# Kernel optimization log

Measured on AMD Instinct MI355X. Metric: run time of the kernel, lower is better.

Reference implementation:

```python
import jax, jax.numpy as jnp
import numpy as np

B, S, D, H = 4, 1024, 1024, 16
DH = D // H
NEG = -10000.0  # mask fill value for non-float32 (bool) masks in the torch code


def setup_inputs() -> dict:
    key = jax.random.key(0)
    ks = jax.random.split(key, 16)
    scale = 0.02
    inp = {
        "query": jax.random.normal(ks[0], (B, S, D), jnp.float32),
        "key": jax.random.normal(ks[1], (B, S, D), jnp.float32),
        "value": jax.random.normal(ks[2], (B, S, D), jnp.float32),
        "pos_embedding": jax.random.normal(ks[3], (B, S, D), jnp.float32),
        # learned params (torch Linear convention: y = x @ W.T + b, W is (out,in))
        "Wq": jax.random.normal(ks[4], (D, D), jnp.float32) * scale,
        "bq": jnp.zeros((D,), jnp.float32),
        "Wk": jax.random.normal(ks[5], (D, D), jnp.float32) * scale,
        "bk": jnp.zeros((D,), jnp.float32),
        "Wv": jax.random.normal(ks[6], (D, D), jnp.float32) * scale,
        "bv": jnp.zeros((D,), jnp.float32),
        "Wpos": jax.random.normal(ks[7], (D, D), jnp.float32) * scale,
        "u_bias": jax.random.normal(ks[8], (H, DH), jnp.float32) * scale,
        "v_bias": jax.random.normal(ks[9], (H, DH), jnp.float32) * scale,
        "Wout": jax.random.normal(ks[10], (D, D), jnp.float32) * scale,
        "bout": jnp.zeros((D,), jnp.float32),
    }
    # right-padding mask: lengths in [S//2, S]; mask[b,i,j] = pad(i) | pad(j)
    lengths = jax.random.randint(ks[11], (B,), S // 2, S + 1)
    pad = jnp.arange(S)[None, :] >= lengths[:, None]  # (B,S)
    inp["mask"] = pad[:, :, None] | pad[:, None, :]  # (B,S,S) bool
    return inp


def _relative_shift(pos_score, mask):
    """Batch-safe Transformer-XL relative shift (vectorized version of the
    per-batch python loop). pos_score: (B,H,S,S), mask: (B,S,S) bool."""
    b, h, s, _ = pos_score.shape
    # per-row true length: S - number of padded rows (column 0 is never padded)
    L = s - jnp.sum(mask[:, :, 0].astype(jnp.int32), axis=-1)  # (B,)
    i = jnp.arange(s)[:, None]
    j = jnp.arange(s)[None, :]

    def shift_one(ps, Lb):  # ps: (H,S,S), Lb: scalar int
        # padded[h,r,0]=0; padded[h,r,k]=ps[h,r,k-1]; flat index of out[i,j] in
        # the (Lb+1, Lb) reshape of padded[:, :Lb, :Lb+1], rows 1: -> offset Lb
        m = Lb + i * Lb + j            # (S,S)
        row = m // (Lb + 1)
        col = m % (Lb + 1)
        g = ps[:, jnp.clip(row, 0, s - 1), jnp.clip(col - 1, 0, s - 1)]  # (H,S,S)
        valid = (i < Lb) & (j < Lb) & (col != 0)
        return jnp.where(valid[None], g, jnp.zeros((), ps.dtype))

    shifted = jax.vmap(shift_one)(pos_score, L)
    # masked_fill_(padding_mask, 0.0)
    return jnp.where(mask[:, None, :, :], jnp.zeros((), pos_score.dtype), shifted)


def reference(query, key, value, pos_embedding, mask,
              Wq, bq, Wk, bk, Wv, bv, Wpos, u_bias, v_bias, Wout, bout):
    b = query.shape[0]
    sqrt_dim = np.sqrt(D).astype(np.float32)

    q = (query @ Wq.T + bq).reshape(b, -1, H, DH)                 # (B,S,H,dh)
    k = (key @ Wk.T + bk).reshape(b, -1, H, DH)                   # (B,S,H,dh)
    v = (value @ Wv.T + bv).reshape(b, -1, H, DH)                 # (B,S,H,dh)
    p = (pos_embedding @ Wpos.T).reshape(b, -1, H, DH)            # (B,S,H,dh)

    content_score = jnp.einsum('bqhd,bkhd->bhqk', q + u_bias, k)  # (B,H,S,S)
    pos_score = jnp.einsum('bqhd,bkhd->bhqk', q + v_bias, p)      # (B,H,S,S)
    pos_score = _relative_shift(pos_score, mask)

    score = (content_score + pos_score) / sqrt_dim
    m4 = mask[:, None, :, :]
    score = jnp.where(m4, NEG, score)
    attn = jax.nn.softmax(score, axis=-1)
    attn = jnp.where(m4, jnp.zeros((), attn.dtype), attn)
    # dropout is identity in eval mode
    context = jnp.einsum('bhqk,bkhd->bqhd', attn, v).reshape(b, -1, D)
    return context @ Wout.T + bout
```

## Files before the change

### kernel.cpp

```cpp
#include <hip/hip_runtime.h>

#define B_ 4
#define S_ 1024
#define D_ 1024
#define H_ 16
#define DH_ 64
#define OOS 0.03125f

#define QPL (1088 * 64)
#define KPL (1024 * 64)
#define VPL (1024 * 64)
#define PPL (200 * 1024)
#define PADLO 1056

#define APL_SW (256 * 32 * 512)
#define WPL_SW (64 * 32 * 512)

typedef __attribute__((ext_vector_type(8))) short short8;
typedef __attribute__((ext_vector_type(4))) float f32x4;
typedef const __attribute__((address_space(1))) unsigned int* gas_t;
typedef __attribute__((address_space(3))) unsigned int* las_t;

__device__ __forceinline__ ushort f2bf(float x) {
  unsigned u = __float_as_uint(x);
  unsigned r = u + 0x7fffu + ((u >> 16) & 1u);
  return (ushort)(r >> 16);
}
__device__ __forceinline__ float bf2f(ushort u) {
  return __uint_as_float(((unsigned)u) << 16);
}

union pack8 { ushort u[8]; uint4 v; };

struct ConvDesc { const float* src; ushort* hi; ushort* lo; };
struct ConvArgs { ConvDesc d[5]; };

__global__ __launch_bounds__(256) void conv_split(ConvArgs args)
{
  const ConvDesc dd = args.d[blockIdx.y];
  const int tt = blockIdx.x;
  const int tid = threadIdx.x;
  const float* src = dd.src + (size_t)tt * 16 * 1024;
  ushort* hi = dd.hi + (size_t)tt * 32 * 512;
  ushort* lo = dd.lo + (size_t)tt * 32 * 512;
#pragma unroll 4
  for (int q = 0; q < 16; ++q) {
    const int s = q * 256 + tid;
    const int r = s >> 8, c4 = s & 255;
    const float4 x = *(const float4*)(src + r * 1024 + c4 * 4);
    const int k = c4 * 4;
    const size_t addr = (size_t)(k >> 5) * 512 + ((k & 31) >> 3) * 128 + r * 8 + (k & 7);
    ushort4 hu, lu;
    hu.x = f2bf(x.x); lu.x = f2bf(x.x - bf2f(hu.x));
    hu.y = f2bf(x.y); lu.y = f2bf(x.y - bf2f(hu.y));
    hu.z = f2bf(x.z); lu.z = f2bf(x.z - bf2f(hu.z));
    hu.w = f2bf(x.w); lu.w = f2bf(x.w - bf2f(hu.w));
    *(ushort4*)(hi + addr) = hu;
    *(ushort4*)(lo + addr) = lu;
  }
}

struct GemmDesc {
  const ushort* Ahi; const ushort* Alo;
  const ushort* Bhi; const ushort* Blo;
  const float* bias; ushort* O1; ushort* O2;
  const float* ub; const float* vb; int mode; int pad;
};
struct GemmArgs { GemmDesc g[4]; };

__global__ __launch_bounds__(256, 2) void gemm_fused(GemmArgs args)
{
  __shared__ __align__(16) ushort SM[16384];
  const GemmDesc g = args.g[blockIdx.z];
  const int tid = threadIdx.x;
  const int wave = tid >> 6, lane = tid & 63;
  const int m16 = lane & 15, quad = lane >> 4;
  const int mw2 = wave & 1, nw2 = wave >> 1;
  const int mt0 = blockIdx.y * 8;
  const int nt0 = blockIdx.x * 8;

  f32x4 acc[4][4];
#pragma unroll
  for (int mf = 0; mf < 4; ++mf)
#pragma unroll
    for (int nf = 0; nf < 4; ++nf) acc[mf][nf] = (f32x4){0.f, 0.f, 0.f, 0.f};

  for (int kb = 0; kb < 32; ++kb) {
    __syncthreads();
    for (int t = wave; t < 32; t += 4) {
      const ushort* gp;
      int l;
      if (t < 8)       { gp = g.Ahi + ((size_t)(mt0 + t) * 32 + kb) * 512;       l = t * 512; }
      else if (t < 16) { gp = g.Alo + ((size_t)(mt0 + t - 8) * 32 + kb) * 512;   l = 4096 + (t - 8) * 512; }
      else if (t < 24) { gp = g.Bhi + ((size_t)(nt0 + t - 16) * 32 + kb) * 512;  l = 8192 + (t - 16) * 512; }
      else             { gp = g.Blo + ((size_t)(nt0 + t - 24) * 32 + kb) * 512;  l = 12288 + (t - 24) * 512; }
      __builtin_amdgcn_global_load_lds((gas_t)(gp + lane * 8), (las_t)(SM + l), 16, 0, 0);
    }
    __syncthreads();
    short8 ah[4], al[4], bh[4], bl[4];
#pragma unroll
    for (int mf = 0; mf < 4; ++mf) {
      ah[mf] = *(const short8*)(SM + (mw2 * 4 + mf) * 512 + lane * 8);
      al[mf] = *(const short8*)(SM + 4096 + (mw2 * 4 + mf) * 512 + lane * 8);
    }
#pragma unroll
    for (int nf = 0; nf < 4; ++nf) {
      bh[nf] = *(const short8*)(SM + 8192 + (nw2 * 4 + nf) * 512 + lane * 8);
      bl[nf] = *(const short8*)(SM + 12288 + (nw2 * 4 + nf) * 512 + lane * 8);
    }
#pragma unroll
    for (int mf = 0; mf < 4; ++mf)
#pragma unroll
      for (int nf = 0; nf < 4; ++nf) {
        acc[mf][nf] = __builtin_amdgcn_mfma_f32_16x16x32_bf16(ah[mf], bh[nf], acc[mf][nf], 0, 0, 0);
        acc[mf][nf] = __builtin_amdgcn_mfma_f32_16x16x32_bf16(ah[mf], bl[nf], acc[mf][nf], 0, 0, 0);
        acc[mf][nf] = __builtin_amdgcn_mfma_f32_16x16x32_bf16(al[mf], bh[nf], acc[mf][nf], 0, 0, 0);
      }
  }

  const int Mb = blockIdx.y * 128, Nb = blockIdx.x * 128;
  float* const E0 = (float*)SM;
  float* const E1 = (float*)(SM + 8192);
#pragma unroll
  for (int p = 0; p < 2; ++p) {
    __syncthreads();
    if (mw2 == p) {
      float* const E = nw2 ? E1 : E0;
#pragma unroll
      for (int mf = 0; mf < 4; ++mf)
#pragma unroll
        for (int nf = 0; nf < 4; ++nf)
#pragma unroll
          for (int reg = 0; reg < 4; ++reg)
            E[(mf * 16 + quad * 4 + reg) * 64 + nf * 16 + m16] = acc[mf][nf][reg];
    }
    __syncthreads();

#pragma unroll
    for (int cpart = 0; cpart < 2; ++cpart) {
      float* const E = cpart ? E1 : E0;
      const int tokBase = Mb + p * 64;
      const int nBase = Nb + cpart * 64;

      if (g.mode == 3) {
#pragma unroll
        for (int q = 0; q < 2; ++q) {
          const int s = tid + 256 * q;
          const int cc = s & 63, rg = s >> 6;
          const int tok0 = tokBase + rg * 8;
          const int n = nBase + cc;
          const int bb = tok0 >> 10, jr = tok0 & 1023;
          const int jt = jr >> 6, ksj = (jr >> 5) & 1, qk = (jr >> 3) & 3;
          const int h = n >> 6, dd = n & 63;
          const int subd = dd >> 4, nn = dd & 15;
          const size_t base = (size_t)(bb * 16 + h) * VPL + (size_t)jt * 4096 +
                              (size_t)(subd * 2 + ksj) * 512 + (qk * 16 + nn) * 8;
          const float bvv = g.bias[n];
          pack8 pk;
#pragma unroll
          for (int i = 0; i < 8; ++i) pk.u[i] = f2bf(E[(rg * 8 + i) * 64 + cc] + bvv);
          *(uint4*)(g.O1 + base) = pk.v;
        }
      } else {
#pragma unroll
        for (int q = 0; q < 2; ++q) {
          const int s = tid + 256 * q;
          const int r = s >> 3, gc = s & 7;
          const int token = tokBase + r;
          const int n = nBase + gc * 8;
          float v[8];
          *(float4*)&v[0] = *(const float4*)&E[r * 64 + gc * 8];
          *(float4*)&v[4] = *(const float4*)&E[r * 64 + gc * 8 + 4];
          if (g.mode == 1) {
            const int bb = token >> 10, sr = token & 1023;
            const int h = n >> 6, d = n & 63;
            const size_t base = (size_t)(bb * 16 + h) * QPL + (size_t)sr * 64 + d;
            pack8 pu, pv;
#pragma unroll
            for (int j = 0; j < 8; ++j) {
              const float qv_ = v[j] + g.bias[n + j];
              pu.u[j] = f2bf(qv_ + g.ub[n + j]);
              pv.u[j] = f2bf(qv_ + g.vb[n + j]);
            }
            *(uint4*)(g.O1 + base) = pu.v;
            *(uint4*)(g.O2 + base) = pv.v;
          } else {
            const int bb = token >> 10, jr = token & 1023;
            const int h = n >> 6, dd = n & 63;
            const int ks = dd >> 5, qk = (dd >> 3) & 3;
            size_t base;
            if (g.mode == 2)
              base = (size_t)(bb * 16 + h) * KPL + (size_t)(jr >> 6) * 4096 +
                     (size_t)((((jr >> 4) & 3) * 2 + ks)) * 512 + (qk * 16 + (jr & 15)) * 8;
            else {
              const int ro = jr + PADLO;
              base = (size_t)(bb * 16 + h) * PPL + (size_t)(ro >> 4) * 1024 +
                     (size_t)ks * 512 + (qk * 16 + (ro & 15)) * 8;
            }
            pack8 pk;
#pragma unroll
            for (int j = 0; j < 8; ++j)
              pk.u[j] = f2bf(v[j] + (g.mode == 2 ? g.bias[n + j] : 0.f));
            *(uint4*)(g.O1 + base) = pk.v;
          }
        }
      }
    }
  }
}

__global__ __launch_bounds__(256, 2) void gemm_out(
    const ushort* __restrict__ Ahi, const ushort* __restrict__ Alo,
    const ushort* __restrict__ Bhi, const ushort* __restrict__ Blo,
    const float* __restrict__ bias, float* __restrict__ C)
{
  __shared__ __align__(16) ushort SM[12288];
  const int tid = threadIdx.x;
  const int wave = tid >> 6, lane = tid & 63;
  const int m16 = lane & 15, quad = lane >> 4;
  const int mw2 = wave & 1, nw2 = wave >> 1;
  const int mt0 = blockIdx.y * 4;
  const int nt0 = blockIdx.x * 8;

  f32x4 acc[2][4];
#pragma unroll
  for (int mf = 0; mf < 2; ++mf)
#pragma unroll
    for (int nf = 0; nf < 4; ++nf) acc[mf][nf] = (f32x4){0.f, 0.f, 0.f, 0.f};

  for (int kb = 0; kb < 32; ++kb) {
    __syncthreads();
    for (int t = wave; t < 24; t += 4) {
      const ushort* g;
      int l;
      if (t < 4)       { g = Ahi + ((size_t)(mt0 + t) * 32 + kb) * 512;      l = t * 512; }
      else if (t < 8)  { g = Alo + ((size_t)(mt0 + t - 4) * 32 + kb) * 512;  l = 2048 + (t - 4) * 512; }
      else if (t < 16) { g = Bhi + ((size_t)(nt0 + t - 8) * 32 + kb) * 512;  l = 4096 + (t - 8) * 512; }
      else             { g = Blo + ((size_t)(nt0 + t - 16) * 32 + kb) * 512; l = 8192 + (t - 16) * 512; }
      __builtin_amdgcn_global_load_lds((gas_t)(g + lane * 8), (las_t)(SM + l), 16, 0, 0);
    }
    __syncthreads();
    short8 ah[2], al[2], bh[4], bl[4];
#pragma unroll
    for (int mf = 0; mf < 2; ++mf) {
      ah[mf] = *(const short8*)(SM + (mw2 * 2 + mf) * 512 + lane * 8);
      al[mf] = *(const short8*)(SM + 2048 + (mw2 * 2 + mf) * 512 + lane * 8);
    }
#pragma unroll
    for (int nf = 0; nf < 4; ++nf) {
      bh[nf] = *(const short8*)(SM + 4096 + (nw2 * 4 + nf) * 512 + lane * 8);
      bl[nf] = *(const short8*)(SM + 8192 + (nw2 * 4 + nf) * 512 + lane * 8);
    }
#pragma unroll
    for (int mf = 0; mf < 2; ++mf)
#pragma unroll
      for (int nf = 0; nf < 4; ++nf) {
        acc[mf][nf] = __builtin_amdgcn_mfma_f32_16x16x32_bf16(ah[mf], bh[nf], acc[mf][nf], 0, 0, 0);
        acc[mf][nf] = __builtin_amdgcn_mfma_f32_16x16x32_bf16(ah[mf], bl[nf], acc[mf][nf], 0, 0, 0);
        acc[mf][nf] = __builtin_amdgcn_mfma_f32_16x16x32_bf16(al[mf], bh[nf], acc[mf][nf], 0, 0, 0);
      }
  }

  const int Mb = blockIdx.y * 64, Nb = blockIdx.x * 128;
  float* const E = (float*)SM;
#pragma unroll
  for (int c = 0; c < 2; ++c) {
    __syncthreads();
    if (nw2 == c) {
#pragma unroll
      for (int mf = 0; mf < 2; ++mf)
#pragma unroll
        for (int nf = 0; nf < 4; ++nf)
#pragma unroll
          for (int reg = 0; reg < 4; ++reg)
            E[(mw2 * 32 + mf * 16 + quad * 4 + reg) * 64 + nf * 16 + m16] = acc[mf][nf][reg];
    }
    __syncthreads();
#pragma unroll
    for (int q = 0; q < 2; ++q) {
      const int s = tid + 256 * q;
      const int r = s >> 3, g = s & 7;
      const int token = Mb + r;
      const int n = Nb + c * 64 + g * 8;
      float v[8];
      *(float4*)&v[0] = *(const float4*)&E[r * 64 + g * 8];
      *(float4*)&v[4] = *(const float4*)&E[r * 64 + g * 8 + 4];
      float4 o0, o1;
      o0.x = v[0] + bias[n + 0]; o0.y = v[1] + bias[n + 1];
      o0.z = v[2] + bias[n + 2]; o0.w = v[3] + bias[n + 3];
      o1.x = v[4] + bias[n + 4]; o1.y = v[5] + bias[n + 5];
      o1.z = v[6] + bias[n + 6]; o1.w = v[7] + bias[n + 7];
      *(float4*)(C + (size_t)token * 1024 + n) = o0;
      *(float4*)(C + (size_t)token * 1024 + n + 4) = o1;
    }
  }
}

__global__ void len_kernel(const int* __restrict__ mask, int* __restrict__ len,
                           ushort* __restrict__ Psw)
{
  const int b = blockIdx.x;
  int cnt = 0;
  for (int i = threadIdx.x; i < S_; i += 256)
    cnt += (mask[(size_t)b * S_ * S_ + (size_t)i * S_] != 0) ? 1 : 0;
  __shared__ int sh[256];
  sh[threadIdx.x] = cnt;
  __syncthreads();
  for (int off = 128; off > 0; off >>= 1) {
    if (threadIdx.x < off) sh[threadIdx.x] += sh[threadIdx.x + off];
    __syncthreads();
  }
  if (threadIdx.x == 0) len[b] = S_ - sh[0];
  for (int idx = threadIdx.x; idx < 16 * 64; idx += 256) {
    const int h = idx >> 6, d = idx & 63;
    Psw[(size_t)(b * 16 + h) * PPL + 65 * 1024 + (d >> 5) * 512 +
        (((d >> 3) & 3) * 16 + 15) * 8 + (d & 7)] = 0;
  }
}

__global__ __launch_bounds__(512, 4) void attn_mfma2(
    const ushort* __restrict__ Qu, const ushort* __restrict__ Qv,
    const ushort* __restrict__ Ksw, const ushort* __restrict__ Vsw,
    const ushort* __restrict__ Psw, const int* __restrict__ len,
    float* __restrict__ CTX)
{
  __shared__ __align__(16) ushort SMEM[26624];
  __shared__ float mrow[64], lrow[64], arow[64];

  ushort* const Ks_  = SMEM;
  ushort* const Vts_ = SMEM + 4096;
  ushort* const P1s_ = SMEM + 8192;
  ushort* const P2s_ = SMEM + 17408;
  float*  const sc   = (float*)(SMEM + 8192);
  ushort* const Pb   = SMEM + 17408;

  const int tid  = threadIdx.x;
  const int wave = tid >> 6, lane = tid & 63;
  const int hw   = wave >> 2, w4 = wave & 3;
  const int m16  = lane & 15, quad = lane >> 4;
  const int mw   = w4 & 1,  nw   = w4 >> 1;
  const int koff0 = quad * 8;

  const int base = blockIdx.x * 64;
  const int i0 = base + hw * 32;
  const int h  = blockIdx.y;
  const int b  = blockIdx.z;
  const int ph = b * 16 + h;
  const int L  = len[b];
  const size_t gb = ((size_t)b * S_) * D_ + h * DH_;

  if (base >= L) {
    for (int idx = tid; idx < 64 * 64; idx += 512) {
      const int r = idx >> 6, d = idx & 63;
      CTX[gb + (size_t)(base + r) * D_ + d] = 0.f;
    }
    return;
  }
  const bool active = (i0 < L);

  const ushort* quP = Qu + (size_t)ph * QPL;
  const ushort* qvP = Qv + (size_t)ph * QPL;
  short8 qufr[2][2], qvfr[2][2][2];
#pragma unroll
  for (int Mt = 0; Mt < 2; ++Mt)
#pragma unroll
    for (int ks = 0; ks < 2; ++ks) {
      qufr[Mt][ks] = *(const short8*)(quP + (size_t)(i0 + 16 * Mt + m16) * 64 + ks * 32 + koff0);
#pragma unroll
      for (int off = 0; off < 2; ++off)
        qvfr[off][Mt][ks] =
            *(const short8*)(qvP + (size_t)(i0 + off + 16 * Mt + m16) * 64 + ks * 32 + koff0);
    }

  if (tid < 64) { mrow[tid] = -3.0e38f; lrow[tid] = 0.f; arow[tid] = 0.f; }

  f32x4 ctx0 = {0.f, 0.f, 0.f, 0.f}, ctx1 = {0.f, 0.f, 0.f, 0.f};

  const ushort* ksP = Ksw + (size_t)ph * KPL;
  const ushort* vsP = Vsw + (size_t)ph * VPL;
  const ushort* psP = Psw + (size_t)ph * PPL;

  for (int j0 = 0; j0 < L; j0 += 64) {
    __syncthreads();

    const int jt = j0 >> 6;
    const int A1 = L - 32 - i0 + j0, A2 = j0 - i0 - 33;
    const int ro1 = A1 + PADLO, ro2 = A2 + PADLO;
    const int rb1 = ro1 >> 4, rb2 = ro2 >> 4;
    const int d1 = ro1 & 15, d2 = ro2 & 15;
    const int rb1lo = (L - 64 - base + j0 + PADLO) >> 4;
    const int rb2lo = (j0 - base - 65 + PADLO) >> 4;
    const ushort* P1h = P1s_ + ((rb1 - rb1lo) << 10);
    const ushort* P2h = P2s_ + ((rb2 - rb2lo) << 10);

    {
      const ushort* kgo = ksP + (size_t)jt * 4096;
      const ushort* vgo = vsP + (size_t)jt * 4096;
      const ushort* p1o = psP + (size_t)rb1lo * 1024;
      const ushort* p2o = psP + (size_t)rb2lo * 1024;
      for (int t = wave; t < 52; t += 8) {
        const ushort* g;
        int l;
        if (t < 8)       { g = kgo + t * 512;        l = t * 512; }
        else if (t < 16) { g = vgo + (t - 8) * 512;  l = 4096 + (t - 8) * 512; }
        else if (t < 34) { g = p1o + (t - 16) * 512; l = 8192 + (t - 16) * 512; }
        else             { g = p2o + (t - 34) * 512; l = 17408 + (t - 34) * 512; }
        __builtin_amdgcn_global_load_lds((gas_t)(g + lane * 8), (las_t)(SMEM + l), 16, 0, 0);
      }
    }
    __syncthreads();

    const int jrem = L - j0;
    const int jmax = (jrem < 64) ? jrem : 64;
    const int cthr = 31 + i0 - j0;

    f32x4 av[9];
#pragma unroll
    for (int t = 0; t < 9; ++t) {
      const int id = w4 + 4 * t;
      f32x4 a = {0.f, 0.f, 0.f, 0.f};
      if (active) {
        if (id < 8) {
          const int Mt = id & 1, Nt = id >> 1;
          if (16 * Nt < jmax) {
            const ushort* bp = Ks_ + (Nt * 2) * 512 + lane * 8;
            a = __builtin_amdgcn_mfma_f32_16x16x32_bf16(qufr[Mt][0], *(const short8*)bp, a, 0, 0, 0);
            a = __builtin_amdgcn_mfma_f32_16x16x32_bf16(qufr[Mt][1], *(const short8*)(bp + 512), a, 0, 0, 0);
          }
        } else if (id < 22) {
          const int e = id - 8, Mt = e & 1, Ntp = e >> 1;
          const int sm = 16 * (Ntp + Mt);
          if (sm >= d1 + 1 && sm <= jmax + d1 + 30 && 16 * Ntp - d1 <= cthr) {
            const ushort* bp = P1h + (Ntp * 2) * 512 + lane * 8;
            a = __builtin_amdgcn_mfma_f32_16x16x32_bf16(qvfr[0][Mt][0], *(const short8*)bp, a, 0, 0, 0);
            a = __builtin_amdgcn_mfma_f32_16x16x32_bf16(qvfr[0][Mt][1], *(const short8*)(bp + 512), a, 0, 0, 0);
          }
        } else {
          const int e = id - 22, Mt = e & 1, Ntp = e >> 1;
          const int sm = 16 * (Ntp + Mt);
          if (sm >= d2 + 1 && sm <= jmax + d2 + 30 && 16 * Ntp + 15 - d2 > cthr) {
            const ushort* bp = P2h + (Ntp * 2) * 512 + lane * 8;
            a = __builtin_amdgcn_mfma_f32_16x16x32_bf16(qvfr[1][Mt][0], *(const short8*)bp, a, 0, 0, 0);
            a = __builtin_amdgcn_mfma_f32_16x16x32_bf16(qvfr[1][Mt][1], *(const short8*)(bp + 512), a, 0, 0, 0);
          }
        }
      }
      av[t] = a;
    }
    __syncthreads();

#pragma unroll
    for (int t = 0; t < 2; ++t) {
      const int id = w4 + 4 * t;
      if (id < 8) {
        const int Mt = id & 1, Nt = id >> 1;
        if (16 * Nt < jmax) {
#pragma unroll
          for (int reg = 0; reg < 4; ++reg)
            sc[(hw * 32 + 16 * Mt + quad * 4 + reg) * 68 + 16 * Nt + m16] =
                active ? av[t][reg] : 0.f;
        }
      }
    }
    __syncthreads();

    if (active) {
#pragma unroll
      for (int t = 0; t < 9; ++t) {
        const int id = w4 + 4 * t;
        if (id >= 8) {
          const bool isG2 = id >= 22;
          const int e = id - (isG2 ? 22 : 8), Mt = e & 1, Ntp = e >> 1;
          const int dl = isG2 ? d2 : d1;
          const int sm = 16 * (Ntp + Mt);
          const bool use = sm >= dl + 1 && sm <= jmax + dl + 30 &&
                           (isG2 ? (16 * Ntp + 15 - dl > cthr) : (16 * Ntp - dl <= cthr));
          if (use) {
            const int c = 16 * Ntp + m16 - dl;
            const bool sel = isG2 ? (c > cthr) : (c <= cthr);
            if (sel) {
#pragma unroll
              for (int reg = 0; reg < 4; ++reg) {
                const int il = 16 * Mt + quad * 4 + reg;
                const int jl = c - 31 + il;
                if (jl >= 0 && jl < 64) sc[(hw * 32 + il) * 68 + jl] += av[t][reg];
              }
            }
          }
        }
      }
    }
    __syncthreads();

    {
      const int row = tid >> 3, t8 = tid & 7, jb = t8 * 8;
      const float* sr = sc + row * 68 + jb;
      float mx = -3.0e38f;
#pragma unroll
      for (int q = 0; q < 8; ++q)
        if (jb + q < jmax) mx = fmaxf(mx, sr[q]);
#pragma unroll
      for (int off = 1; off < 8; off <<= 1)
        mx = fmaxf(mx, __shfl_xor(mx, off, 64));
      if (t8 == 0) {
        const float mo = mrow[row];
        const float mn = fmaxf(mo, mx);
        arow[row] = __expf((mo - mn) * OOS);
        mrow[row] = mn;
      }
    }
    __syncthreads();
    {
      const int row = tid >> 3, t8 = tid & 7, jb = t8 * 8;
      const float m = mrow[row];
      const float* sr = sc + row * 68 + jb;
      float e[8], s = 0.f;
#pragma unroll
      for (int q = 0; q < 8; ++q) {
        float v = 0.f;
        if (jb + q < jmax) v = __expf((sr[q] - m) * OOS);
        e[q] = v;
        s += v;
      }
      ushort4 u0, u1;
      u0.x = f2bf(e[0]); u0.y = f2bf(e[1]); u0.z = f2bf(e[2]); u0.w = f2bf(e[3]);
      u1.x = f2bf(e[4]); u1.y = f2bf(e[5]); u1.z = f2bf(e[6]); u1.w = f2bf(e[7]);
      *(ushort4*)&Pb[row * 72 + jb] = u0;
      *(ushort4*)&Pb[row * 72 + jb + 4] = u1;
#pragma unroll
      for (int off = 1; off < 8; off <<= 1) s += __shfl_xor(s, off, 64);
      if (t8 == 0) lrow[row] = lrow[row] * arow[row] + s;
    }
    __syncthreads();

    if (active) {
      float al[4];
#pragma unroll
      for (int reg = 0; reg < 4; ++reg) al[reg] = arow[hw * 32 + 16 * mw + quad * 4 + reg];
#pragma unroll
      for (int reg = 0; reg < 4; ++reg) { ctx0[reg] *= al[reg]; ctx1[reg] *= al[reg]; }
      const ushort* ap = Pb + (hw * 32 + 16 * mw + m16) * 72;
#pragma unroll
      for (int ksj = 0; ksj < 2; ++ksj) {
        const short8 a = *(const short8*)(ap + ksj * 32 + koff0);
        ctx0 = __builtin_amdgcn_mfma_f32_16x16x32_bf16(
            a, *(const short8*)(Vts_ + ((nw * 2) * 2 + ksj) * 512 + lane * 8), ctx0, 0, 0, 0);
        ctx1 = __builtin_amdgcn_mfma_f32_16x16x32_bf16(
            a, *(const short8*)(Vts_ + ((nw * 2 + 1) * 2 + ksj) * 512 + lane * 8), ctx1, 0, 0, 0);
      }
    }
  }

#pragma unroll
  for (int reg = 0; reg < 4; ++reg) {
    const int il = 16 * mw + quad * 4 + reg;
    const int gi = i0 + il;
    const float inv = (active && gi < L) ? (1.f / lrow[hw * 32 + il]) : 0.f;
    CTX[gb + (size_t)gi * D_ + nw * 32 + m16]      = ctx0[reg] * inv;
    CTX[gb + (size_t)gi * D_ + nw * 32 + 16 + m16] = ctx1[reg] * inv;
  }
}

extern "C" void kernel_launch(void* const* d_in, const int* in_sizes, int n_in,
                              void* d_out, int out_size, void* d_ws, size_t ws_size,
                              hipStream_t stream)
{
  (void)in_sizes; (void)n_in; (void)out_size;
  const float* query = (const float*)d_in[0];
  const float* key   = (const float*)d_in[1];
  const float* value = (const float*)d_in[2];
  const float* pos   = (const float*)d_in[3];
  const float* Wq    = (const float*)d_in[4];
  const float* bq    = (const float*)d_in[5];
  const float* Wk    = (const float*)d_in[6];
  const float* bk    = (const float*)d_in[7];
  const float* Wv    = (const float*)d_in[8];
  const float* bv    = (const float*)d_in[9];
  const float* Wpos  = (const float*)d_in[10];
  const float* ub    = (const float*)d_in[11];
  const float* vb    = (const float*)d_in[12];
  const float* Wout  = (const float*)d_in[13];
  const float* bout  = (const float*)d_in[14];
  const int*   mask  = (const int*)d_in[15];

  char* cur = (char*)d_ws;
  auto take = [&](size_t bytes) {
    char* p = cur;
    cur += (bytes + 255) & ~(size_t)255;
    return p;
  };
  float*  CTX = (float*)take((size_t)4096 * 1024 * 4);
  ushort* Qu  = (ushort*)take((size_t)64 * QPL * 2);
  ushort* Qv  = (ushort*)take((size_t)64 * QPL * 2);
  ushort* Ksw = (ushort*)take((size_t)64 * KPL * 2);
  ushort* Vsw = (ushort*)take((size_t)64 * VPL * 2);
  ushort* Psw = (ushort*)take((size_t)64 * PPL * 2);
  ushort* Ah[4], *Al[4];
  for (int i = 0; i < 4; ++i) {
    Ah[i] = (ushort*)take((size_t)APL_SW * 2);
    Al[i] = (ushort*)take((size_t)APL_SW * 2);
  }
  ushort* Wh[5], *Wl[5];
  for (int i = 0; i < 5; ++i) {
    Wh[i] = (ushort*)take((size_t)WPL_SW * 2);
    Wl[i] = (ushort*)take((size_t)WPL_SW * 2);
  }
  int* len = (int*)take(256);
  ushort* Ch = Ah[0];
  ushort* Cl = Al[0];
  if (ws_size < (size_t)(cur - (char*)d_ws)) return;

  len_kernel<<<dim3(B_), dim3(256), 0, stream>>>(mask, len, Psw);

  {
    ConvArgs a;
    a.d[0] = {query, Ah[0], Al[0]};
    a.d[1] = {key,   Ah[1], Al[1]};
    a.d[2] = {value, Ah[2], Al[2]};
    a.d[3] = {pos,   Ah[3], Al[3]};
    a.d[4] = {query, Ah[0], Al[0]};
    conv_split<<<dim3(256, 4), dim3(256), 0, stream>>>(a);
    ConvArgs w;
    w.d[0] = {Wq,   Wh[0], Wl[0]};
    w.d[1] = {Wk,   Wh[1], Wl[1]};
    w.d[2] = {Wv,   Wh[2], Wl[2]};
    w.d[3] = {Wpos, Wh[3], Wl[3]};
    w.d[4] = {Wout, Wh[4], Wl[4]};
    conv_split<<<dim3(64, 5), dim3(256), 0, stream>>>(w);
  }

  {
    GemmArgs ga;
    ga.g[0] = {Ah[0], Al[0], Wh[0], Wl[0], bq, Qu, Qv, ub, vb, 1, 0};
    ga.g[1] = {Ah[1], Al[1], Wh[1], Wl[1], bk, Ksw, nullptr, nullptr, nullptr, 2, 0};
    ga.g[2] = {Ah[2], Al[2], Wh[2], Wl[2], bv, Vsw, nullptr, nullptr, nullptr, 3, 0};
    ga.g[3] = {Ah[3], Al[3], Wh[3], Wl[3], nullptr, Psw, nullptr, nullptr, nullptr, 4, 0};
    gemm_fused<<<dim3(8, 32, 4), dim3(256), 0, stream>>>(ga);
  }

  attn_mfma2<<<dim3(S_ / 64, H_, B_), dim3(512), 0, stream>>>(
      Qu, Qv, Ksw, Vsw, Psw, len, CTX);

  {
    ConvArgs c;
    c.d[0] = {CTX, Ch, Cl};
    c.d[1] = c.d[0]; c.d[2] = c.d[0]; c.d[3] = c.d[0]; c.d[4] = c.d[0];
    conv_split<<<dim3(256, 1), dim3(256), 0, stream>>>(c);
  }

  gemm_out<<<dim3(8, 64), dim3(256), 0, stream>>>(Ch, Cl, Wh[4], Wl[4], bout,
                                                  (float*)d_out);
}
```

Before: 675.1 us.

## Prefetch next K/V/P tile into LDS during softmax of current tile

The attention kernel now starts the global-to-LDS loads for the next key block right after the score MFMAs, so those loads overlap the score scatter, softmax and PV phases. V fragments are read into registers before the buffer is overwritten. The score and probability scratch buffers move to a separate LDS region so they do not collide with the in-flight tile. Plain __syncthreads are replaced with explicit barriers that wait only on LDS ops, except one that also waits on vector memory. The cost is more LDS per block (about 80KB instead of 53KB), which may reduce the number of resident blocks per CU.

After: 718.0 us. 1.06x slower.

```diff
diff --git a/kernel.cpp b/kernel.cpp
--- a/kernel.cpp
+++ b/kernel.cpp
@@ -31,6 +31,19 @@
 }
 
 union pack8 { ushort u[8]; uint4 v; };
+
+__device__ __forceinline__ void bar_lgkm() {
+  __builtin_amdgcn_sched_barrier(0);
+  asm volatile("s_waitcnt lgkmcnt(0)" ::: "memory");
+  __builtin_amdgcn_s_barrier();
+  __builtin_amdgcn_sched_barrier(0);
+}
+__device__ __forceinline__ void bar_all() {
+  __builtin_amdgcn_sched_barrier(0);
+  asm volatile("s_waitcnt vmcnt(0) lgkmcnt(0)" ::: "memory");
+  __builtin_amdgcn_s_barrier();
+  __builtin_amdgcn_sched_barrier(0);
+}
 
 struct ConvDesc { const float* src; ushort* hi; ushort* lo; };
 struct ConvArgs { ConvDesc d[5]; };
@@ -324,15 +337,15 @@
     const ushort* __restrict__ Psw, const int* __restrict__ len,
     float* __restrict__ CTX)
 {
-  __shared__ __align__(16) ushort SMEM[26624];
+  __shared__ __align__(16) ushort SMEM[39936];
   __shared__ float mrow[64], lrow[64], arow[64];
 
   ushort* const Ks_  = SMEM;
   ushort* const Vts_ = SMEM + 4096;
   ushort* const P1s_ = SMEM + 8192;
   ushort* const P2s_ = SMEM + 17408;
-  float*  const sc   = (float*)(SMEM + 8192);
-  ushort* const Pb   = SMEM + 17408;
+  float*  const sc   = (float*)(SMEM + 26624);
+  ushort* const Pb   = SMEM + 35328;
 
   const int tid  = threadIdx.x;
   const int wave = tid >> 6, lane = tid & 63;
@@ -358,6 +371,31 @@
   }
   const bool active = (i0 < L);
 
+  const ushort* ksP = Ksw + (size_t)ph * KPL;
+  const ushort* vsP = Vsw + (size_t)ph * VPL;
+  const ushort* psP = Psw + (size_t)ph * PPL;
+
+  auto issue_stage = [&](int j0s) {
+    const int jts = j0s >> 6;
+    const int rb1s = (L - 64 - base + j0s + PADLO) >> 4;
+    const int rb2s = (j0s - base - 65 + PADLO) >> 4;
+    const ushort* kgo = ksP + (size_t)jts * 4096;
+    const ushort* vgo = vsP + (size_t)jts * 4096;
+    const ushort* p1o = psP + (size_t)rb1s * 1024;
+    const ushort* p2o = psP + (size_t)rb2s * 1024;
+    for (int t = wave; t < 52; t += 8) {
+      const ushort* g;
+      int l;
+      if (t < 8)       { g = kgo + t * 512;        l = t * 512; }
+      else if (t < 16) { g = vgo + (t - 8) * 512;  l = 4096 + (t - 8) * 512; }
+      else if (t < 34) { g = p1o + (t - 16) * 512; l = 8192 + (t - 16) * 512; }
+      else             { g = p2o + (t - 34) * 512; l = 17408 + (t - 34) * 512; }
+      __builtin_amdgcn_global_load_lds((gas_t)(g + lane * 8), (las_t)(SMEM + l), 16, 0, 0);
+    }
+  };
+
+  issue_stage(0);
+
   const ushort* quP = Qu + (size_t)ph * QPL;
   const ushort* qvP = Qv + (size_t)ph * QPL;
   short8 qufr[2][2], qvfr[2][2][2];
@@ -376,14 +414,7 @@
 
   f32x4 ctx0 = {0.f, 0.f, 0.f, 0.f}, ctx1 = {0.f, 0.f, 0.f, 0.f};
 
-  const ushort* ksP = Ksw + (size_t)ph * KPL;
-  const ushort* vsP = Vsw + (size_t)ph * VPL;
-  const ushort* psP = Psw + (size_t)ph * PPL;
-
   for (int j0 = 0; j0 < L; j0 += 64) {
-    __syncthreads();
-
-    const int jt = j0 >> 6;
     const int A1 = L - 32 - i0 + j0, A2 = j0 - i0 - 33;
     const int ro1 = A1 + PADLO, ro2 = A2 + PADLO;
     const int rb1 = ro1 >> 4, rb2 = ro2 >> 4;
@@ -393,26 +424,20 @@
     const ushort* P1h = P1s_ + ((rb1 - rb1lo) << 10);
     const ushort* P2h = P2s_ + ((rb2 - rb2lo) << 10);
 
-    {
-      const ushort* kgo = ksP + (size_t)jt * 4096;
-      const ushort* vgo = vsP + (size_t)jt * 4096;
-      const ushort* p1o = psP + (size_t)rb1lo * 1024;
-      const ushort* p2o = psP + (size_t)rb2lo * 1024;
-      for (int t = wave; t < 52; t += 8) {
-        const ushort* g;
-        int l;
-        if (t < 8)       { g = kgo + t * 512;        l = t * 512; }
-        else if (t < 16) { g = vgo + (t - 8) * 512;  l = 4096 + (t - 8) * 512; }
-        else if (t < 34) { g = p1o + (t - 16) * 512; l = 8192 + (t - 16) * 512; }
-        else             { g = p2o + (t - 34) * 512; l = 17408 + (t - 34) * 512; }
-        __builtin_amdgcn_global_load_lds((gas_t)(g + lane * 8), (las_t)(SMEM + l), 16, 0, 0);
-      }
-    }
-    __syncthreads();
+    bar_all();
 
     const int jrem = L - j0;
     const int jmax = (jrem < 64) ? jrem : 64;
     const int cthr = 31 + i0 - j0;
+
+    short8 vreg0, vreg1, vreg2, vreg3;
+    if (active) {
+      const ushort* vb0 = Vts_ + (nw * 4) * 512 + lane * 8;
+      vreg0 = *(const short8*)(vb0);
+      vreg1 = *(const short8*)(vb0 + 512);
+      vreg2 = *(const short8*)(vb0 + 1024);
+      vreg3 = *(const short8*)(vb0 + 1536);
+    }
 
     f32x4 av[9];
 #pragma unroll
@@ -447,7 +472,9 @@
       }
       av[t] = a;
     }
-    __syncthreads();
+    bar_lgkm();
+
+    if (j0 + 64 < L) issue_stage(j0 + 64);
 
 #pragma unroll
     for (int t = 0; t < 2; ++t) {
@@ -462,7 +489,7 @@
         }
       }
     }
-    __syncthreads();
+    bar_lgkm();
 
     if (active) {
 #pragma unroll
@@ -490,7 +517,7 @@
         }
       }
     }
-    __syncthreads();
+    bar_lgkm();
 
     {
       const int row = tid >> 3, t8 = tid & 7, jb = t8 * 8;
@@ -509,7 +536,7 @@
         mrow[row] = mn;
       }
     }
-    __syncthreads();
+    bar_lgkm();
     {
       const int row = tid >> 3, t8 = tid & 7, jb = t8 * 8;
       const float m = mrow[row];
@@ -531,7 +558,7 @@
       for (int off = 1; off < 8; off <<= 1) s += __shfl_xor(s, off, 64);
       if (t8 == 0) lrow[row] = lrow[row] * arow[row] + s;
     }
-    __syncthreads();
+    bar_lgkm();
 
     if (active) {
       float al[4];
@@ -540,14 +567,12 @@
 #pragma unroll
       for (int reg = 0; reg < 4; ++reg) { ctx0[reg] *= al[reg]; ctx1[reg] *= al[reg]; }
       const ushort* ap = Pb + (hw * 32 + 16 * mw + m16) * 72;
-#pragma unroll
-      for (int ksj = 0; ksj < 2; ++ksj) {
-        const short8 a = *(const short8*)(ap + ksj * 32 + koff0);
-        ctx0 = __builtin_amdgcn_mfma_f32_16x16x32_bf16(
-            a, *(const short8*)(Vts_ + ((nw * 2) * 2 + ksj) * 512 + lane * 8), ctx0, 0, 0, 0);
-        ctx1 = __builtin_amdgcn_mfma_f32_16x16x32_bf16(
-            a, *(const short8*)(Vts_ + ((nw * 2 + 1) * 2 + ksj) * 512 + lane * 8), ctx1, 0, 0, 0);
-      }
+      const short8 a0 = *(const short8*)(ap + koff0);
+      const short8 a1 = *(const short8*)(ap + 32 + koff0);
+      ctx0 = __builtin_amdgcn_mfma_f32_16x16x32_bf16(a0, vreg0, ctx0, 0, 0, 0);
+      ctx0 = __builtin_amdgcn_mfma_f32_16x16x32_bf16(a1, vreg1, ctx0, 0, 0, 0);
+      ctx1 = __builtin_amdgcn_mfma_f32_16x16x32_bf16(a0, vreg2, ctx1, 0, 0, 0);
+      ctx1 = __builtin_amdgcn_mfma_f32_16x16x32_bf16(a1, vreg3, ctx1, 0, 0, 0);
     }
   }
 
```
